# Kernel optimization log

Hardware: AMD Instinct MI355X
Metric: run time of the kernel (lower is better)

Reference implementation:

```python
import jax, jax.numpy as jnp
import numpy as np

LN_EPS = 1e-5

def _ln(x, g, b):
    mu = jnp.mean(x, axis=-1, keepdims=True)
    var = jnp.mean((x - mu) ** 2, axis=-1, keepdims=True)
    return (x - mu) * jax.lax.rsqrt(var + LN_EPS) * g + b

def _gelu(x):
    return jax.nn.gelu(x, approximate=False)

def _time_embed(t, dim):
    # standard sinusoidal embedding on scalar times t: (B,) -> (B, dim)
    half = dim // 2
    freqs = jnp.exp(-jnp.log(10000.0) * jnp.arange(half, dtype=jnp.float32) / max(half - 1, 1))
    ang = t[:, None] * freqs[None, :]
    return jnp.concatenate([jnp.sin(ang), jnp.cos(ang)], axis=-1)

def setup_inputs() -> dict:
    key = jax.random.key(0)
    B, D, C, H, M = 1024, 128, 256, 512, 64
    ks = jax.random.split(key, 24)
    w = lambda k, shp: jax.random.normal(k, shp, dtype=jnp.float32) * 0.02
    inp = {
        "noise": jax.random.normal(ks[0], (B, D), dtype=jnp.float32),
        "context": jax.random.normal(ks[1], (B, C), dtype=jnp.float32),
        "support_memory": jax.random.normal(ks[2], (B, M, D), dtype=jnp.float32),
        "num_steps": 4,
        # memory adapter: LayerNorm(D) + Linear(D->H)
        "mem_ln_g": jnp.ones((D,), jnp.float32), "mem_ln_b": jnp.zeros((D,), jnp.float32),
        "Wa": w(ks[3], (D, H)), "ba": jnp.zeros((H,), jnp.float32),
        # attention projections H->H
        "Wq": w(ks[4], (H, H)), "bq": jnp.zeros((H,), jnp.float32),
        "Wk": w(ks[5], (H, H)), "bk": jnp.zeros((H,), jnp.float32),
        "Wv": w(ks[6], (H, H)), "bv": jnp.zeros((H,), jnp.float32),
        "Wo": w(ks[7], (H, H)), "bo": jnp.zeros((H,), jnp.float32),
        # particle proj: LN(D) + Linear(D->H) + GELU + Linear(H->H)
        "pp_ln_g": jnp.ones((D,), jnp.float32), "pp_ln_b": jnp.zeros((D,), jnp.float32),
        "Wp1": w(ks[8], (D, H)), "bp1": jnp.zeros((H,), jnp.float32),
        "Wp2": w(ks[9], (H, H)), "bp2": jnp.zeros((H,), jnp.float32),
        # context proj C->H
        "Wc": w(ks[10], (C, H)), "bc": jnp.zeros((H,), jnp.float32),
        # time proj H->H (on sinusoidal embedding of dim H)
        "Wt": w(ks[11], (H, H)), "bt": jnp.zeros((H,), jnp.float32),
        # fusion head: LN(4H) + Linear(4H->H) + GELU + Linear(H->D)
        "f_ln_g": jnp.ones((4 * H,), jnp.float32), "f_ln_b": jnp.zeros((4 * H,), jnp.float32),
        "Wf1": w(ks[12], (4 * H, H)), "bf1": jnp.zeros((H,), jnp.float32),
        "Wf2": w(ks[13], (H, D)), "bf2": jnp.zeros((D,), jnp.float32),
    }
    return inp

def reference(noise, context, support_memory, num_steps,
              mem_ln_g, mem_ln_b, Wa, ba,
              Wq, bq, Wk, bk, Wv, bv, Wo, bo,
              pp_ln_g, pp_ln_b, Wp1, bp1, Wp2, bp2,
              Wc, bc, Wt, bt,
              f_ln_g, f_ln_b, Wf1, bf1, Wf2, bf2):
    B, D = noise.shape
    H = Wq.shape[0]
    heads = 4
    dh = H // heads
    scale = dh ** -0.5

    # encode support memory once (solver-invariant), like encode_memory()
    enc = _ln(support_memory, mem_ln_g, mem_ln_b) @ Wa + ba            # (B, M, H)
    M = enc.shape[1]
    k_mem = (enc @ Wk + bk).reshape(B, M, heads, dh)                    # (B, M, h, dh)
    v_mem = (enc @ Wv + bv).reshape(B, M, heads, dh)
    ctx_h = context @ Wc + bc                                           # (B, H)

    def velocity(y, t):
        te = _time_embed(t, H) @ Wt + bt                                # (B, H)
        h = _gelu(_ln(y, pp_ln_g, pp_ln_b) @ Wp1 + bp1) @ Wp2 + bp2      # (B, H)
        q = (h @ Wq + bq).reshape(B, heads, dh)
        logits = jnp.einsum('bhd,bmhd->bhm', q, k_mem) * scale
        attn = jax.nn.softmax(logits, axis=-1)
        summ = jnp.einsum('bhm,bmhd->bhd', attn, v_mem).reshape(B, H)
        m = summ @ Wo + bo                                              # (B, H)
        z = jnp.concatenate([h, m, ctx_h, te], axis=-1)                 # (B, 4H)
        return _gelu(_ln(z, f_ln_g, f_ln_b) @ Wf1 + bf1) @ Wf2 + bf2     # (B, D)

    dt = 1.0 / float(num_steps)
    t0s = jnp.arange(num_steps, dtype=jnp.float32) * dt

    def heun_step(y, t0):
        tb0 = jnp.full((B,), t0, dtype=y.dtype)
        k1 = velocity(y, tb0)
        k2 = velocity(y + dt * k1, tb0 + dt)
        return y + 0.5 * dt * (k1 + k2), None

    y_final, _ = jax.lax.scan(heun_step, noise, t0s)
    return y_final
```

## Files before the change

### kernel.cpp

```cpp
#include <hip/hip_runtime.h>
#include <hip/hip_bf16.h>
#include <cstdint>
#include <cstddef>

#define LN_EPS 1e-5f

typedef __attribute__((ext_vector_type(8))) short short8;
typedef __attribute__((ext_vector_type(4))) float f32x4;

__device__ __forceinline__ float gelu_exact(float x) {
  return 0.5f * x * (1.0f + erff(x * 0.70710678118654752440f));
}
__device__ __forceinline__ float bflo(unsigned int x) {
  union { unsigned int i; float f; } v; v.i = x << 16; return v.f;
}
__device__ __forceinline__ float bfhi(unsigned int x) {
  union { unsigned int i; float f; } v; v.i = x & 0xffff0000u; return v.f;
}
__device__ __forceinline__ float bf2f(short s) {
  union { unsigned int i; float f; } v; v.i = ((unsigned int)(unsigned short)s) << 16; return v.f;
}
__device__ __forceinline__ short bf16s(float f) {
  __hip_bfloat16 h = __float2bfloat16(f);
  return *reinterpret_cast<short*>(&h);
}

__global__ __launch_bounds__(256) void ln_bf16_k(const float* __restrict__ X,
                                                 const float* __restrict__ KIN, float a,
                                                 const float* __restrict__ g,
                                                 const float* __restrict__ bb,
                                                 __hip_bfloat16* __restrict__ out, int rows) {
  int row = blockIdx.x * 4 + (threadIdx.x >> 6);
  if (row >= rows) return;
  int l = threadIdx.x & 63;
  size_t base = (size_t)row * 128;
  float x0 = X[base + l], x1 = X[base + l + 64];
  if (KIN) { x0 += a * KIN[base + l]; x1 += a * KIN[base + l + 64]; }
  float s = x0 + x1;
#pragma unroll
  for (int o = 32; o > 0; o >>= 1) s += __shfl_xor(s, o);
  float mu = s * (1.0f / 128.0f);
  float d0 = x0 - mu, d1 = x1 - mu;
  float v = d0 * d0 + d1 * d1;
#pragma unroll
  for (int o = 32; o > 0; o >>= 1) v += __shfl_xor(v, o);
  float rstd = rsqrtf(v * (1.0f / 128.0f) + LN_EPS);
  out[base + l] = __float2bfloat16(d0 * rstd * g[l] + bb[l]);
  out[base + l + 64] = __float2bfloat16(d1 * rstd * g[l + 64] + bb[l + 64]);
}

template <int ROWS, int BN, bool GELU_OUT, bool OUT_BF16>
__global__ __launch_bounds__(ROWS * 4) void gemm_mfma_k(
    const short* __restrict__ A, const short* __restrict__ WT,
    const float* __restrict__ bias, void* __restrict__ Cout,
    int K, int lda, int ldw, int ldc, float alpha,
    int hsA, int hsB, long hsC) {
  constexpr int T = ROWS * 4;
  constexpr int NFRAG = BN / 16;
  constexpr int NB = (BN * 8) / T;
  __shared__ __align__(16) short As[2][ROWS][72];
  __shared__ __align__(16) short Bs[2][BN][72];
  A += (size_t)blockIdx.z * hsA;
  WT += (size_t)blockIdx.z * hsB;
  const size_t cOff = (size_t)blockIdx.z * (size_t)hsC;
  const int tid = threadIdx.x;
  const int w = tid >> 6, l = tid & 63;
  const int row0 = blockIdx.y * ROWS, col0 = blockIdx.x * BN;
  f32x4 acc[NFRAG];
#pragma unroll
  for (int i = 0; i < NFRAG; ++i) acc[i] = (f32x4){0.f, 0.f, 0.f, 0.f};

  const int nt = K >> 6;
  short8 aR0, aR1;
  short8 bR[NB];
  auto loadA = [&](int t) {
    int k0 = t * 64;
    int c1 = tid + T;
    aR0 = *(const short8*)(A + (size_t)(row0 + (tid >> 3)) * lda + k0 + (tid & 7) * 8);
    aR1 = *(const short8*)(A + (size_t)(row0 + (c1 >> 3)) * lda + k0 + (c1 & 7) * 8);
  };
  auto loadB = [&](int t) {
    int k0 = t * 64;
#pragma unroll
    for (int i = 0; i < NB; ++i) {
      int c = tid + i * T;
      bR[i] = *(const short8*)(WT + (size_t)(col0 + (c >> 3)) * ldw + k0 + (c & 7) * 8);
    }
  };
  auto storeT = [&](int buf) {
    int c1 = tid + T;
    *(short8*)&As[buf][tid >> 3][(tid & 7) * 8] = aR0;
    *(short8*)&As[buf][c1 >> 3][(c1 & 7) * 8] = aR1;
#pragma unroll
    for (int i = 0; i < NB; ++i) {
      int c = tid + i * T;
      *(short8*)&Bs[buf][c >> 3][(c & 7) * 8] = bR[i];
    }
  };

  loadA(0);
  loadB(0);
  for (int t = 0; t < nt; ++t) {
    int buf = t & 1;
    storeT(buf);
    __syncthreads();
    if (t + 1 < nt) { loadA(t + 1); loadB(t + 1); }
    short8 af0 = *(const short8*)&As[buf][w * 16 + (l & 15)][(l >> 4) * 8];
    short8 af1 = *(const short8*)&As[buf][w * 16 + (l & 15)][(l >> 4) * 8 + 32];
#pragma unroll
    for (int nc = 0; nc < NFRAG; ++nc) {
      short8 bf0 = *(const short8*)&Bs[buf][nc * 16 + (l & 15)][(l >> 4) * 8];
      acc[nc] = __builtin_amdgcn_mfma_f32_16x16x32_bf16(af0, bf0, acc[nc], 0, 0, 0);
      short8 bf1 = *(const short8*)&Bs[buf][nc * 16 + (l & 15)][(l >> 4) * 8 + 32];
      acc[nc] = __builtin_amdgcn_mfma_f32_16x16x32_bf16(af1, bf1, acc[nc], 0, 0, 0);
    }
    __syncthreads();
  }
  const int cr = (l >> 4) * 4;
  const int cc = l & 15;
#pragma unroll
  for (int nc = 0; nc < NFRAG; ++nc) {
    int gc = col0 + nc * 16 + cc;
    float bv = bias ? bias[gc] : 0.0f;
#pragma unroll
    for (int r = 0; r < 4; ++r) {
      int gr = row0 + w * 16 + cr + r;
      float v = acc[nc][r] * alpha + bv;
      if (GELU_OUT) v = gelu_exact(v);
      if (OUT_BF16)
        ((__hip_bfloat16*)Cout)[cOff + (size_t)gr * ldc + gc] = __float2bfloat16(v);
      else
        ((float*)Cout)[cOff + (size_t)gr * ldc + gc] = v;
    }
  }
}

__global__ __launch_bounds__(256) void gemm_heun_k(
    const short* __restrict__ A, const short* __restrict__ WT,
    const float* __restrict__ bias, const float* __restrict__ yin,
    const float* __restrict__ kaux, float c0, float* __restrict__ outY) {
  __shared__ __align__(16) short As[2][64][72];
  __shared__ __align__(16) short Bs[2][32][72];
  const int tid = threadIdx.x;
  const int w = tid >> 6, l = tid & 63;
  const int row0 = blockIdx.y * 64, col0 = blockIdx.x * 32;
  f32x4 acc[2];
  acc[0] = (f32x4){0.f, 0.f, 0.f, 0.f};
  acc[1] = (f32x4){0.f, 0.f, 0.f, 0.f};
  short8 aR0, aR1, bR;
  auto loadA = [&](int t) {
    int k0 = t * 64;
    int c1 = tid + 256;
    aR0 = *(const short8*)(A + (size_t)(row0 + (tid >> 3)) * 512 + k0 + (tid & 7) * 8);
    aR1 = *(const short8*)(A + (size_t)(row0 + (c1 >> 3)) * 512 + k0 + (c1 & 7) * 8);
  };
  auto loadB = [&](int t) {
    int k0 = t * 64;
    bR = *(const short8*)(WT + (size_t)(col0 + (tid >> 3)) * 512 + k0 + (tid & 7) * 8);
  };
  auto storeT = [&](int buf) {
    int c1 = tid + 256;
    *(short8*)&As[buf][tid >> 3][(tid & 7) * 8] = aR0;
    *(short8*)&As[buf][c1 >> 3][(c1 & 7) * 8] = aR1;
    *(short8*)&Bs[buf][tid >> 3][(tid & 7) * 8] = bR;
  };
  loadA(0);
  loadB(0);
  for (int t = 0; t < 8; ++t) {
    int buf = t & 1;
    storeT(buf);
    __syncthreads();
    if (t + 1 < 8) { loadA(t + 1); loadB(t + 1); }
    short8 af0 = *(const short8*)&As[buf][w * 16 + (l & 15)][(l >> 4) * 8];
    short8 af1 = *(const short8*)&As[buf][w * 16 + (l & 15)][(l >> 4) * 8 + 32];
#pragma unroll
    for (int nc = 0; nc < 2; ++nc) {
      short8 bf0 = *(const short8*)&Bs[buf][nc * 16 + (l & 15)][(l >> 4) * 8];
      acc[nc] = __builtin_amdgcn_mfma_f32_16x16x32_bf16(af0, bf0, acc[nc], 0, 0, 0);
      short8 bf1 = *(const short8*)&Bs[buf][nc * 16 + (l & 15)][(l >> 4) * 8 + 32];
      acc[nc] = __builtin_amdgcn_mfma_f32_16x16x32_bf16(af1, bf1, acc[nc], 0, 0, 0);
    }
    __syncthreads();
  }
  const int cr = (l >> 4) * 4, cc = l & 15;
#pragma unroll
  for (int nc = 0; nc < 2; ++nc) {
    int gc = col0 + nc * 16 + cc;
    float bv = bias[gc];
#pragma unroll
    for (int r = 0; r < 4; ++r) {
      int gr = row0 + w * 16 + cr + r;
      float v = acc[nc][r] + bv;
      size_t idx = (size_t)gr * 128 + gc;
      outY[idx] = yin[idx] + c0 * (kaux[idx] + v);
    }
  }
}

struct TCBatch { const float* src[5]; short* dst[5]; };
__global__ __launch_bounds__(256) void transpose_cast_batch_k(TCBatch p) {
  const float* W = p.src[blockIdx.z];
  short* WT = p.dst[blockIdx.z];
  __shared__ float tile[64][65];
  int n0 = blockIdx.x * 64, k0 = blockIdx.y * 64;
#pragma unroll
  for (int i = 0; i < 16; ++i) {
    int e = threadIdx.x + i * 256;
    int r = e >> 6, c = e & 63;
    tile[r][c] = W[(size_t)(k0 + r) * 512 + n0 + c];
  }
  __syncthreads();
#pragma unroll
  for (int i = 0; i < 16; ++i) {
    int e = threadIdx.x + i * 256;
    int r = e >> 6, c = e & 63;
    WT[(size_t)(n0 + r) * 512 + k0 + c] = bf16s(tile[c][r]);
  }
}

__global__ __launch_bounds__(256) void transpose_cast_k(const float* __restrict__ W,
                                                        short* __restrict__ WT,
                                                        int K, int N) {
  __shared__ float tile[64][65];
  int n0 = blockIdx.x * 64, k0 = blockIdx.y * 64;
#pragma unroll
  for (int i = 0; i < 16; ++i) {
    int e = threadIdx.x + i * 256;
    int r = e >> 6, c = e & 63;
    tile[r][c] = W[(size_t)(k0 + r) * N + n0 + c];
  }
  __syncthreads();
#pragma unroll
  for (int i = 0; i < 16; ++i) {
    int e = threadIdx.x + i * 256;
    int r = e >> 6, c = e & 63;
    WT[(size_t)(n0 + r) * K + k0 + c] = bf16s(tile[c][r]);
  }
}

__global__ void cast_bf16_k(const float* __restrict__ src, short* __restrict__ dst, int n) {
  int i = blockIdx.x * blockDim.x + threadIdx.x;
  if (i < n) dst[i] = bf16s(src[i]);
}

__global__ __launch_bounds__(256) void bias_fuse_k(const float* __restrict__ va,
                                                   const float* __restrict__ Wx,
                                                   const float* __restrict__ bx,
                                                   float* __restrict__ out) {
  const int tid = threadIdx.x;
  const int j = blockIdx.x * 32 + (tid >> 3);
  const int kl = tid & 7;
  float s = 0.f;
  for (int k = kl; k < 512; k += 8) s += va[k] * Wx[(size_t)k * 512 + j];
  s += __shfl_xor(s, 1);
  s += __shfl_xor(s, 2);
  s += __shfl_xor(s, 4);
  if (kl == 0) out[j] = s + bx[j];
}

__global__ __launch_bounds__(256) void bqp_k(const float* __restrict__ bhqq,
                                             const short* __restrict__ Wak_bf,
                                             float scale, float* __restrict__ bqp) {
  const int tid = threadIdx.x;
  const int j = blockIdx.x * 32 + (tid >> 3);
  const int h = j >> 7, e = j & 127;
  const int kl = tid & 7;
  float s = 0.f;
  for (int d = kl; d < 128; d += 8)
    s += bhqq[h * 128 + d] * bf2f(Wak_bf[(size_t)e * 512 + h * 128 + d]);
  s += __shfl_xor(s, 1);
  s += __shfl_xor(s, 2);
  s += __shfl_xor(s, 4);
  if (kl == 0) bqp[j] = s * scale;
}

__global__ __launch_bounds__(512) void te_k(const float* __restrict__ Wt,
                                            const float* __restrict__ bt,
                                            float* __restrict__ te) {
  __shared__ float emb[512];
  const int ci = blockIdx.x;
  const float t = 0.25f * (float)((ci >> 1) + (ci & 1));
  const int j = threadIdx.x;
  if (j < 256) {
    float fr = expf(-9.210340371976184f * (float)j * (1.0f / 255.0f));
    float ang = t * fr;
    emb[j] = sinf(ang);
    emb[j + 256] = cosf(ang);
  }
  __syncthreads();
  float s0 = 0.f, s1 = 0.f, s2 = 0.f, s3 = 0.f;
  for (int k = 0; k < 512; k += 4) {
    s0 += emb[k] * Wt[(size_t)k * 512 + j];
    s1 += emb[k + 1] * Wt[(size_t)(k + 1) * 512 + j];
    s2 += emb[k + 2] * Wt[(size_t)(k + 2) * 512 + j];
    s3 += emb[k + 3] * Wt[(size_t)(k + 3) * 512 + j];
  }
  te[(size_t)ci * 512 + j] = bt[j] + ((s0 + s1) + (s2 + s3));
}

__global__ __launch_bounds__(256) void attn_k(const __hip_bfloat16* __restrict__ hq,
                                              const short* __restrict__ lnsm,
                                              __hip_bfloat16* __restrict__ sctx) {
  const int b = blockIdx.x;
  const int tid = threadIdx.x;
  const int w = tid >> 6, l = tid & 63;
  __shared__ __align__(16) short smt[64 * 128];
  __shared__ float qs[512];
  __shared__ float att[4][64];
  {
    unsigned int u = ((const unsigned int*)(hq + (size_t)b * 1024 + 512))[tid];
    qs[2 * tid] = bflo(u);
    qs[2 * tid + 1] = bfhi(u);
  }
  {
    const int m = tid >> 2;
    const short* src = lnsm + ((size_t)b * 64 + m) * 128;
#pragma unroll
    for (int j = 0; j < 4; ++j) {
      int c = (tid & 3) + 4 * j;
      short8 v = *(const short8*)(src + c * 8);
      *(short8*)&smt[m * 128 + ((c ^ (m & 7)) * 8)] = v;
    }
  }
  __syncthreads();
  const float* qh = qs + w * 128;
  float acc = 0.f;
#pragma unroll
  for (int i = 0; i < 16; ++i) {
    uint4 u = *(const uint4*)&smt[l * 128 + ((i ^ (l & 7)) * 8)];
    const int d = i * 8;
    acc += bflo(u.x) * qh[d + 0] + bfhi(u.x) * qh[d + 1] +
           bflo(u.y) * qh[d + 2] + bfhi(u.y) * qh[d + 3] +
           bflo(u.z) * qh[d + 4] + bfhi(u.z) * qh[d + 5] +
           bflo(u.w) * qh[d + 6] + bfhi(u.w) * qh[d + 7];
  }
  float mx = acc;
#pragma unroll
  for (int o = 32; o > 0; o >>= 1) mx = fmaxf(mx, __shfl_xor(mx, o));
  float e = expf(acc - mx);
  float se = e;
#pragma unroll
  for (int o = 32; o > 0; o >>= 1) se += __shfl_xor(se, o);
  att[w][l] = e / se;
  const int cb = l >> 2, doff = 2 * (l & 3);
  float a0 = 0.f, a1 = 0.f;
#pragma unroll 8
  for (int m = 0; m < 64; ++m) {
    float am = att[w][m];
    unsigned int u = *(const unsigned int*)&smt[m * 128 + ((cb ^ (m & 7)) * 8) + doff];
    a0 += am * bflo(u);
    a1 += am * bfhi(u);
  }
  unsigned int pr = ((unsigned int)(unsigned short)bf16s(a1) << 16) |
                    (unsigned int)(unsigned short)bf16s(a0);
  ((unsigned int*)(sctx + (size_t)b * 512 + w * 128))[l] = pr;
}

__global__ __launch_bounds__(512) void zln_k(const __hip_bfloat16* __restrict__ hq,
                                             const __hip_bfloat16* __restrict__ mo,
                                             const __hip_bfloat16* __restrict__ ctxh,
                                             const float* __restrict__ te_row,
                                             const float* __restrict__ g,
                                             const float* __restrict__ bb,
                                             __hip_bfloat16* __restrict__ zout) {
  const int b = blockIdx.x;
  const int tid = threadIdx.x;
  float v0 = __bfloat162float(hq[(size_t)b * 1024 + tid]);
  float v1 = __bfloat162float(mo[(size_t)b * 512 + tid]);
  float v2 = __bfloat162float(ctxh[(size_t)b * 512 + tid]);
  float v3 = te_row[tid];
  __shared__ float red[8];
  float s = v0 + v1 + v2 + v3;
#pragma unroll
  for (int o = 32; o > 0; o >>= 1) s += __shfl_xor(s, o);
  if ((tid & 63) == 0) red[tid >> 6] = s;
  __syncthreads();
  s = red[0] + red[1] + red[2] + red[3] + red[4] + red[5] + red[6] + red[7];
  float mu = s * (1.0f / 2048.0f);
  float d0 = v0 - mu, d1 = v1 - mu, d2 = v2 - mu, d3 = v3 - mu;
  float vv = d0 * d0 + d1 * d1 + d2 * d2 + d3 * d3;
  __syncthreads();
#pragma unroll
  for (int o = 32; o > 0; o >>= 1) vv += __shfl_xor(vv, o);
  if ((tid & 63) == 0) red[tid >> 6] = vv;
  __syncthreads();
  vv = red[0] + red[1] + red[2] + red[3] + red[4] + red[5] + red[6] + red[7];
  float rstd = rsqrtf(vv * (1.0f / 2048.0f) + LN_EPS);
  zout[(size_t)b * 2048 + tid] = __float2bfloat16(d0 * rstd * g[tid] + bb[tid]);
  zout[(size_t)b * 2048 + 512 + tid] = __float2bfloat16(d1 * rstd * g[512 + tid] + bb[512 + tid]);
  zout[(size_t)b * 2048 + 1024 + tid] = __float2bfloat16(d2 * rstd * g[1024 + tid] + bb[1024 + tid]);
  zout[(size_t)b * 2048 + 1536 + tid] = __float2bfloat16(d3 * rstd * g[1536 + tid] + bb[1536 + tid]);
}

extern "C" void kernel_launch(void* const* d_in, const int* in_sizes, int n_in,
                              void* d_out, int out_size, void* d_ws, size_t ws_size,
                              hipStream_t stream) {
  (void)in_sizes; (void)n_in; (void)out_size; (void)ws_size;
  const int B = 1024, Mm = 64;
  const int BMrows = B * Mm;
  const float ATTN_SCALE = 0.08838834764831845f;
  const size_t SL = (size_t)512 * 512;

  const float* noise = (const float*)d_in[0];
  const float* context = (const float*)d_in[1];
  const float* sm = (const float*)d_in[2];
  const float* mem_ln_g = (const float*)d_in[4];
  const float* mem_ln_b = (const float*)d_in[5];
  const float* Wa = (const float*)d_in[6];
  const float* ba = (const float*)d_in[7];
  const float* Wq = (const float*)d_in[8];
  const float* bq = (const float*)d_in[9];
  const float* Wk = (const float*)d_in[10];
  const float* bk = (const float*)d_in[11];
  (void)bk;
  const float* Wv = (const float*)d_in[12];
  const float* bv = (const float*)d_in[13];
  const float* Wo = (const float*)d_in[14];
  const float* bo = (const float*)d_in[15];
  const float* pp_ln_g = (const float*)d_in[16];
  const float* pp_ln_b = (const float*)d_in[17];
  const float* Wp1 = (const float*)d_in[18];
  const float* bp1 = (const float*)d_in[19];
  const float* Wp2 = (const float*)d_in[20];
  const float* bp2 = (const float*)d_in[21];
  const float* Wc = (const float*)d_in[22];
  const float* bc = (const float*)d_in[23];
  const float* Wt = (const float*)d_in[24];
  const float* bt = (const float*)d_in[25];
  const float* f_ln_g = (const float*)d_in[26];
  const float* f_ln_b = (const float*)d_in[27];
  const float* Wf1 = (const float*)d_in[28];
  const float* bf1 = (const float*)d_in[29];
  const float* Wf2 = (const float*)d_in[30];
  const float* bf2 = (const float*)d_in[31];
  float* out = (float*)d_out;

  char* wsb = (char*)d_ws;
  size_t off = 0;
  auto alloc = [&](size_t bytes) -> void* {
    off = (off + 255) & ~(size_t)255;
    void* p = wsb + off;
    off += bytes;
    return p;
  };
  short* lnsm = (short*)alloc((size_t)BMrows * 128 * 2);
  short* T512 = (short*)alloc(4 * SL * 2);
  short* WkT = T512;
  short* WvT = T512 + SL;
  short* WqT = T512 + 2 * SL;
  short* WoT = T512 + 3 * SL;
  short* Wp1T = (short*)alloc((size_t)512 * 128 * 2);
  short* WhqT = (short*)alloc((size_t)1024 * 512 * 2);
  short* WfoldT = (short*)alloc(SL * 2);
  short* WcT = (short*)alloc((size_t)512 * 256 * 2);
  short* Wf1T = (short*)alloc((size_t)512 * 2048 * 2);
  short* Wf2T = (short*)alloc((size_t)128 * 512 * 2);
  short* WaB = (short*)alloc((size_t)128 * 512 * 2);
  short* Wp2B = (short*)alloc(SL * 2);
  short* WakavB = (short*)alloc(2 * (size_t)128 * 512 * 2);
  short* Wak_bf = WakavB;
  short* Wav_bf = WakavB + (size_t)128 * 512;
  short* Wp2q_bf = (short*)alloc(SL * 2);
  float* bhq = (float*)alloc(1024 * 4);
  float* bofold = (float*)alloc(512 * 4);
  float* bhqq = (float*)alloc(512 * 4);
  float* bav = (float*)alloc(512 * 4);
  float* te_table = (float*)alloc(8 * 512 * 4);
  short* ctxh = (short*)alloc((size_t)B * 512 * 2);
  float* k1 = (float*)alloc((size_t)B * 128 * 4);
  float* ybuf = (float*)alloc((size_t)B * 128 * 4);
  short* ctxb = (short*)alloc((size_t)B * 256 * 2);
  short* yln = (short*)alloc((size_t)B * 128 * 2);
  short* hmid = (short*)alloc((size_t)B * 512 * 2);
  short* hqbuf = (short*)alloc((size_t)B * 1024 * 2);
  short* sctx = (short*)alloc((size_t)B * 512 * 2);
  short* mobuf = (short*)alloc((size_t)B * 512 * 2);
  short* zbuf = (short*)alloc((size_t)B * 2048 * 2);
  short* fmid = (short*)alloc((size_t)B * 512 * 2);

  ln_bf16_k<<<BMrows / 4, 256, 0, stream>>>(sm, nullptr, 0.f, mem_ln_g, mem_ln_b,
                                            (__hip_bfloat16*)lnsm, BMrows);
  cast_bf16_k<<<(128 * 512 + 255) / 256, 256, 0, stream>>>(Wa, WaB, 128 * 512);
  cast_bf16_k<<<(512 * 512 + 255) / 256, 256, 0, stream>>>(Wp2, Wp2B, 512 * 512);
  cast_bf16_k<<<(B * 256 + 255) / 256, 256, 0, stream>>>(context, ctxb, B * 256);
  {
    TCBatch p;
    p.src[0] = Wk; p.src[1] = Wv; p.src[2] = Wq; p.src[3] = Wo; p.src[4] = Wp2;
    p.dst[0] = WkT; p.dst[1] = WvT; p.dst[2] = WqT; p.dst[3] = WoT; p.dst[4] = WhqT;
    transpose_cast_batch_k<<<dim3(8, 8, 5), 256, 0, stream>>>(p);
  }
  transpose_cast_k<<<dim3(8, 2), 256, 0, stream>>>(Wp1, Wp1T, 128, 512);
  transpose_cast_k<<<dim3(8, 4), 256, 0, stream>>>(Wc, WcT, 256, 512);
  transpose_cast_k<<<dim3(8, 32), 256, 0, stream>>>(Wf1, Wf1T, 2048, 512);
  transpose_cast_k<<<dim3(2, 8), 256, 0, stream>>>(Wf2, Wf2T, 512, 128);
  gemm_mfma_k<64, 64, false, true><<<dim3(8, 2, 2), 256, 0, stream>>>(
      WaB, WkT, nullptr, WakavB, 512, 512, 512, 512, 1.f, 0, (int)SL, 128 * 512);
  gemm_mfma_k<64, 64, false, true><<<dim3(8, 8), 256, 0, stream>>>(
      Wp2B, WqT, nullptr, Wp2q_bf, 512, 512, 512, 512, 1.f, 0, 0, 0);
  gemm_mfma_k<64, 64, false, true><<<dim3(8, 2, 4), 256, 0, stream>>>(
      Wak_bf, Wp2q_bf, nullptr, WhqT + SL, 128, 512, 512, 512, ATTN_SCALE,
      128, 128, 128 * 512);
  gemm_mfma_k<64, 64, false, true><<<dim3(2, 8, 4), 256, 0, stream>>>(
      WoT, Wav_bf, nullptr, WfoldT, 128, 512, 512, 512, 1.f, 128, 128, 128);
  bias_fuse_k<<<16, 256, 0, stream>>>(bp2, Wq, bq, bhqq);
  bqp_k<<<16, 256, 0, stream>>>(bhqq, Wak_bf, ATTN_SCALE, bhq + 512);
  hipMemcpyAsync(bhq, bp2, 512 * 4, hipMemcpyDeviceToDevice, stream);
  bias_fuse_k<<<16, 256, 0, stream>>>(ba, Wv, bv, bav);
  bias_fuse_k<<<16, 256, 0, stream>>>(bav, Wo, bo, bofold);
  gemm_mfma_k<64, 64, false, true><<<dim3(8, 16), 256, 0, stream>>>(
      ctxb, WcT, bc, ctxh, 256, 256, 256, 512, 1.f, 0, 0, 0);
  te_k<<<8, 512, 0, stream>>>(Wt, bt, te_table);

  const float dt = 0.25f;
  auto chain = [&](const float* ycur, const float* kin, float a, int tidx) {
    ln_bf16_k<<<B / 4, 256, 0, stream>>>(ycur, kin, a, pp_ln_g, pp_ln_b,
                                         (__hip_bfloat16*)yln, B);
    gemm_mfma_k<32, 32, true, true><<<dim3(16, 32), 128, 0, stream>>>(
        yln, Wp1T, bp1, hmid, 128, 128, 128, 512, 1.f, 0, 0, 0);
    gemm_mfma_k<32, 64, false, true><<<dim3(16, 32), 128, 0, stream>>>(
        hmid, WhqT, bhq, hqbuf, 512, 512, 512, 1024, 1.f, 0, 0, 0);
    attn_k<<<B, 256, 0, stream>>>((const __hip_bfloat16*)hqbuf, lnsm,
                                  (__hip_bfloat16*)sctx);
    gemm_mfma_k<32, 32, false, true><<<dim3(16, 32), 128, 0, stream>>>(
        sctx, WfoldT, bofold, mobuf, 512, 512, 512, 512, 1.f, 0, 0, 0);
    zln_k<<<B, 512, 0, stream>>>((const __hip_bfloat16*)hqbuf, (const __hip_bfloat16*)mobuf,
                                 (const __hip_bfloat16*)ctxh, te_table + (size_t)tidx * 512,
                                 f_ln_g, f_ln_b, (__hip_bfloat16*)zbuf);
    gemm_mfma_k<32, 32, true, true><<<dim3(16, 32), 128, 0, stream>>>(
        zbuf, Wf1T, bf1, fmid, 2048, 2048, 2048, 512, 1.f, 0, 0, 0);
  };

  const float* ycur = noise;
  for (int s = 0; s < 4; ++s) {
    chain(ycur, nullptr, 0.f, 2 * s);
    gemm_mfma_k<32, 32, false, false><<<dim3(4, 32), 128, 0, stream>>>(
        fmid, Wf2T, bf2, k1, 512, 512, 512, 128, 1.f, 0, 0, 0);
    chain(ycur, k1, dt, 2 * s + 1);
    float* ynext = (s == 3) ? out : ybuf;
    gemm_heun_k<<<dim3(4, 16), 256, 0, stream>>>(
        fmid, Wf2T, bf2, ycur, k1, 0.5f * dt, ynext);
    ycur = ybuf;
  }
}
```

Measured before the change: 589.6 us.

## Fuse fusion-head LayerNorm into the Wf1 GEMM A-operand load

Removes the separate zln_k kernel and the z buffer write/read by computing per-row LayerNorm statistics inside the Wf1 GEMM and normalizing the A operand on the fly from hq, mo, ctx and the time-embedding row. Variance is computed as E[x^2]-mu^2 in one pass, and each 32-row block recomputes stats (16x redundant across column blocks) and reloads unnormalized bf16 data with extra ALU per tile. This trades one launch and a 4MB round trip per chain for redundant stats reads and more per-tile load work.

```diff
diff --git a/kernel.cpp b/kernel.cpp
--- a/kernel.cpp
+++ b/kernel.cpp
@@ -135,6 +135,142 @@
   }
 }
 
+__global__ __launch_bounds__(128) void zgemm_k(
+    const short* __restrict__ hq, const short* __restrict__ mo,
+    const short* __restrict__ ctx, const float* __restrict__ te_row,
+    const float* __restrict__ zg, const float* __restrict__ zb,
+    const short* __restrict__ WT, const float* __restrict__ bias,
+    short* __restrict__ outC) {
+  __shared__ __align__(16) short As[2][32][72];
+  __shared__ __align__(16) short Bs[2][32][72];
+  __shared__ float muS[32], rsS[32];
+  const int tid = threadIdx.x;
+  const int w = tid >> 6, l = tid & 63;
+  const int row0 = blockIdx.y * 32, col0 = blockIdx.x * 32;
+  {
+    const int r = tid >> 2, q = tid & 3;
+    const short* ph = hq + (size_t)(row0 + r) * 1024 + q * 128;
+    const short* pm = mo + (size_t)(row0 + r) * 512 + q * 128;
+    const short* pc = ctx + (size_t)(row0 + r) * 512 + q * 128;
+    float s = 0.f, s2 = 0.f;
+#pragma unroll 4
+    for (int i = 0; i < 16; ++i) {
+      short8 a = *(const short8*)(ph + i * 8);
+      short8 b = *(const short8*)(pm + i * 8);
+      short8 c = *(const short8*)(pc + i * 8);
+#pragma unroll
+      for (int j = 0; j < 8; ++j) {
+        float fa = bf2f(a[j]), fb = bf2f(b[j]), fc = bf2f(c[j]);
+        s += fa + fb + fc;
+        s2 += fa * fa + fb * fb + fc * fc;
+      }
+    }
+    const float* pt = te_row + q * 128;
+#pragma unroll 8
+    for (int i = 0; i < 32; ++i) {
+      float4 v = *(const float4*)(pt + i * 4);
+      s += v.x + v.y + v.z + v.w;
+      s2 += v.x * v.x + v.y * v.y + v.z * v.z + v.w * v.w;
+    }
+    s += __shfl_xor(s, 1); s += __shfl_xor(s, 2);
+    s2 += __shfl_xor(s2, 1); s2 += __shfl_xor(s2, 2);
+    if (q == 0) {
+      float mu = s * (1.0f / 2048.0f);
+      muS[r] = mu;
+      rsS[r] = rsqrtf(s2 * (1.0f / 2048.0f) - mu * mu + LN_EPS);
+    }
+  }
+  __syncthreads();
+
+  const int rA0 = tid >> 3, rA1 = (tid + 128) >> 3, kc = (tid & 7) * 8;
+  const float mu0 = muS[rA0], rs0 = rsS[rA0];
+  const float mu1 = muS[rA1], rs1 = rsS[rA1];
+
+  f32x4 acc[2];
+  acc[0] = (f32x4){0.f, 0.f, 0.f, 0.f};
+  acc[1] = (f32x4){0.f, 0.f, 0.f, 0.f};
+  short8 aR0, aR1;
+  short8 bR[2];
+  auto loadA = [&](int t) {
+    const int k = t * 64 + kc;
+    float f0[8], f1[8];
+    if (k < 1536) {
+      const short* src; int stride, koff;
+      if (k < 512)       { src = hq;  stride = 1024; koff = k; }
+      else if (k < 1024) { src = mo;  stride = 512;  koff = k - 512; }
+      else               { src = ctx; stride = 512;  koff = k - 1024; }
+      short8 a = *(const short8*)(src + (size_t)(row0 + rA0) * stride + koff);
+      short8 b = *(const short8*)(src + (size_t)(row0 + rA1) * stride + koff);
+#pragma unroll
+      for (int j = 0; j < 8; ++j) { f0[j] = bf2f(a[j]); f1[j] = bf2f(b[j]); }
+    } else {
+      const float* pt = te_row + (k - 1536);
+      float4 v0 = *(const float4*)pt, v1 = *(const float4*)(pt + 4);
+      f0[0] = v0.x; f0[1] = v0.y; f0[2] = v0.z; f0[3] = v0.w;
+      f0[4] = v1.x; f0[5] = v1.y; f0[6] = v1.z; f0[7] = v1.w;
+#pragma unroll
+      for (int j = 0; j < 8; ++j) f1[j] = f0[j];
+    }
+    float4 g0 = *(const float4*)(zg + k), g1 = *(const float4*)(zg + k + 4);
+    float4 b0 = *(const float4*)(zb + k), b1 = *(const float4*)(zb + k + 4);
+    float gv[8] = {g0.x, g0.y, g0.z, g0.w, g1.x, g1.y, g1.z, g1.w};
+    float bv[8] = {b0.x, b0.y, b0.z, b0.w, b1.x, b1.y, b1.z, b1.w};
+#pragma unroll
+    for (int j = 0; j < 8; ++j) {
+      aR0[j] = bf16s((f0[j] - mu0) * rs0 * gv[j] + bv[j]);
+      aR1[j] = bf16s((f1[j] - mu1) * rs1 * gv[j] + bv[j]);
+    }
+  };
+  auto loadB = [&](int t) {
+    int k0 = t * 64;
+#pragma unroll
+    for (int i = 0; i < 2; ++i) {
+      int c = tid + i * 128;
+      bR[i] = *(const short8*)(WT + (size_t)(col0 + (c >> 3)) * 2048 + k0 + (c & 7) * 8);
+    }
+  };
+  auto storeT = [&](int buf) {
+    int c1 = tid + 128;
+    *(short8*)&As[buf][tid >> 3][(tid & 7) * 8] = aR0;
+    *(short8*)&As[buf][c1 >> 3][(c1 & 7) * 8] = aR1;
+#pragma unroll
+    for (int i = 0; i < 2; ++i) {
+      int c = tid + i * 128;
+      *(short8*)&Bs[buf][c >> 3][(c & 7) * 8] = bR[i];
+    }
+  };
+
+  loadA(0);
+  loadB(0);
+  for (int t = 0; t < 32; ++t) {
+    int buf = t & 1;
+    storeT(buf);
+    __syncthreads();
+    if (t + 1 < 32) { loadA(t + 1); loadB(t + 1); }
+    short8 af0 = *(const short8*)&As[buf][w * 16 + (l & 15)][(l >> 4) * 8];
+    short8 af1 = *(const short8*)&As[buf][w * 16 + (l & 15)][(l >> 4) * 8 + 32];
+#pragma unroll
+    for (int nc = 0; nc < 2; ++nc) {
+      short8 bf0 = *(const short8*)&Bs[buf][nc * 16 + (l & 15)][(l >> 4) * 8];
+      acc[nc] = __builtin_amdgcn_mfma_f32_16x16x32_bf16(af0, bf0, acc[nc], 0, 0, 0);
+      short8 bf1 = *(const short8*)&Bs[buf][nc * 16 + (l & 15)][(l >> 4) * 8 + 32];
+      acc[nc] = __builtin_amdgcn_mfma_f32_16x16x32_bf16(af1, bf1, acc[nc], 0, 0, 0);
+    }
+    __syncthreads();
+  }
+  const int cr = (l >> 4) * 4, cc = l & 15;
+#pragma unroll
+  for (int nc = 0; nc < 2; ++nc) {
+    int gc = col0 + nc * 16 + cc;
+    float bv = bias[gc];
+#pragma unroll
+    for (int r = 0; r < 4; ++r) {
+      int gr = row0 + w * 16 + cr + r;
+      outC[(size_t)gr * 512 + gc] = bf16s(gelu_exact(acc[nc][r] + bv));
+    }
+  }
+}
+
 __global__ __launch_bounds__(256) void gemm_heun_k(
     const short* __restrict__ A, const short* __restrict__ WT,
     const float* __restrict__ bias, const float* __restrict__ yin,
@@ -354,42 +490,6 @@
   unsigned int pr = ((unsigned int)(unsigned short)bf16s(a1) << 16) |
                     (unsigned int)(unsigned short)bf16s(a0);
   ((unsigned int*)(sctx + (size_t)b * 512 + w * 128))[l] = pr;
-}
-
-__global__ __launch_bounds__(512) void zln_k(const __hip_bfloat16* __restrict__ hq,
-                                             const __hip_bfloat16* __restrict__ mo,
-                                             const __hip_bfloat16* __restrict__ ctxh,
-                                             const float* __restrict__ te_row,
-                                             const float* __restrict__ g,
-                                             const float* __restrict__ bb,
-                                             __hip_bfloat16* __restrict__ zout) {
-  const int b = blockIdx.x;
-  const int tid = threadIdx.x;
-  float v0 = __bfloat162float(hq[(size_t)b * 1024 + tid]);
-  float v1 = __bfloat162float(mo[(size_t)b * 512 + tid]);
-  float v2 = __bfloat162float(ctxh[(size_t)b * 512 + tid]);
-  float v3 = te_row[tid];
-  __shared__ float red[8];
-  float s = v0 + v1 + v2 + v3;
-#pragma unroll
-  for (int o = 32; o > 0; o >>= 1) s += __shfl_xor(s, o);
-  if ((tid & 63) == 0) red[tid >> 6] = s;
-  __syncthreads();
-  s = red[0] + red[1] + red[2] + red[3] + red[4] + red[5] + red[6] + red[7];
-  float mu = s * (1.0f / 2048.0f);
-  float d0 = v0 - mu, d1 = v1 - mu, d2 = v2 - mu, d3 = v3 - mu;
-  float vv = d0 * d0 + d1 * d1 + d2 * d2 + d3 * d3;
-  __syncthreads();
-#pragma unroll
-  for (int o = 32; o > 0; o >>= 1) vv += __shfl_xor(vv, o);
-  if ((tid & 63) == 0) red[tid >> 6] = vv;
-  __syncthreads();
-  vv = red[0] + red[1] + red[2] + red[3] + red[4] + red[5] + red[6] + red[7];
-  float rstd = rsqrtf(vv * (1.0f / 2048.0f) + LN_EPS);
-  zout[(size_t)b * 2048 + tid] = __float2bfloat16(d0 * rstd * g[tid] + bb[tid]);
-  zout[(size_t)b * 2048 + 512 + tid] = __float2bfloat16(d1 * rstd * g[512 + tid] + bb[512 + tid]);
-  zout[(size_t)b * 2048 + 1024 + tid] = __float2bfloat16(d2 * rstd * g[1024 + tid] + bb[1024 + tid]);
-  zout[(size_t)b * 2048 + 1536 + tid] = __float2bfloat16(d3 * rstd * g[1536 + tid] + bb[1536 + tid]);
 }
 
 extern "C" void kernel_launch(void* const* d_in, const int* in_sizes, int n_in,
@@ -475,7 +575,6 @@
   short* hqbuf = (short*)alloc((size_t)B * 1024 * 2);
   short* sctx = (short*)alloc((size_t)B * 512 * 2);
   short* mobuf = (short*)alloc((size_t)B * 512 * 2);
-  short* zbuf = (short*)alloc((size_t)B * 2048 * 2);
   short* fmid = (short*)alloc((size_t)B * 512 * 2);
 
   ln_bf16_k<<<BMrows / 4, 256, 0, stream>>>(sm, nullptr, 0.f, mem_ln_g, mem_ln_b,
@@ -523,11 +622,9 @@
                                   (__hip_bfloat16*)sctx);
     gemm_mfma_k<32, 32, false, true><<<dim3(16, 32), 128, 0, stream>>>(
         sctx, WfoldT, bofold, mobuf, 512, 512, 512, 512, 1.f, 0, 0, 0);
-    zln_k<<<B, 512, 0, stream>>>((const __hip_bfloat16*)hqbuf, (const __hip_bfloat16*)mobuf,
-                                 (const __hip_bfloat16*)ctxh, te_table + (size_t)tidx * 512,
-                                 f_ln_g, f_ln_b, (__hip_bfloat16*)zbuf);
-    gemm_mfma_k<32, 32, true, true><<<dim3(16, 32), 128, 0, stream>>>(
-        zbuf, Wf1T, bf1, fmid, 2048, 2048, 2048, 512, 1.f, 0, 0, 0);
+    zgemm_k<<<dim3(16, 32), 128, 0, stream>>>(
+        hqbuf, mobuf, ctxh, te_table + (size_t)tidx * 512, f_ln_g, f_ln_b,
+        Wf1T, bf1, fmid);
   };
 
   const float* ycur = noise;
```

Result: slower. 745.9 us (+26.5%).
